# Optimization experiments

Measured on AMD Instinct MI355X. Metric: run time of the kernel, lower is better.

The kernel has to match this reference:

```python
import math
import jax, jax.numpy as jnp
import numpy as np

DIM = 1024
QK_DIM = 200
HIDDEN = 2 * DIM  # expansion_factor = 2
N = 8192


def setup_inputs() -> dict:
    key = jax.random.key(0)
    ks = jax.random.split(key, 8)
    s = 0.02
    return {
        "x": jax.random.normal(ks[0], (N, DIM), dtype=jnp.float32),
        "W_hidden": jax.random.normal(ks[1], (DIM, 2 * HIDDEN), dtype=jnp.float32) * s,
        "b_hidden": jnp.zeros((2 * HIDDEN,), dtype=jnp.float32),
        "W_qk": jax.random.normal(ks[2], (DIM, QK_DIM), dtype=jnp.float32) * s,
        "b_qk": jnp.zeros((QK_DIM,), dtype=jnp.float32),
        "gamma": 1.0 + jax.random.normal(ks[3], (2, QK_DIM), dtype=jnp.float32) * s,
        "beta": jnp.zeros((2, QK_DIM), dtype=jnp.float32),
        "W_out": jax.random.normal(ks[4], (HIDDEN, DIM), dtype=jnp.float32) * s,
        "b_out": jnp.zeros((DIM,), dtype=jnp.float32),
    }


def reference(x, W_hidden, b_hidden, W_qk, b_qk, gamma, beta, W_out, b_out):
    # to_hidden: Linear(dim -> 2*hidden) + SiLU, then chunk into v, gate
    hid = jax.nn.silu(x @ W_hidden + b_hidden)        # [N, 2H]
    v, gate = jnp.split(hid, 2, axis=-1)              # [N, H] each
    # to_qk: Linear(dim -> qk_dim) + SiLU
    qk = jax.nn.silu(x @ W_qk + b_qk)                 # [N, qk]
    # OffsetScale (heads=2): per-head affine on the shared qk
    q = qk * gamma[0] + beta[0]                       # [N, qk]
    k = qk * gamma[1] + beta[1]                       # [N, qk]
    # scores scaled by sqrt(dim) (module uses self.dim, not qk_dim)
    sim = (q @ k.T) * (1.0 / math.sqrt(x.shape[-1]))  # [N, N]
    # ReLU-squared attention (no softmax); dropout=0.0 -> identity
    attn = jnp.square(jax.nn.relu(sim))
    out = attn @ v                                    # [N, H]
    out = out * gate
    out = out @ W_out + b_out                         # [N, dim]
    # add_residual=True in this module multiplies by x
    return out * x
```

## Files before the change

kernel.cpp:

```cpp
#include <hip/hip_runtime.h>
#include <stdint.h>


typedef __bf16 bf16x8 __attribute__((ext_vector_type(8)));
typedef float f32x4 __attribute__((ext_vector_type(4)));

__device__ __forceinline__ uint16_t f2bf(float f) {
  uint32_t u = __builtin_bit_cast(uint32_t, f);
  u += 0x7fffu + ((u >> 16) & 1u);
  return (uint16_t)(u >> 16);
}
__device__ __forceinline__ float silu_f(float s) {
  return s / (1.f + __expf(-s));
}

__device__ __forceinline__ void gload16(const void* g, void* l) {
  __builtin_amdgcn_global_load_lds(
      (__attribute__((address_space(1))) void*)const_cast<void*>(g),
      (__attribute__((address_space(3))) void*)l, 16, 0, 0);
}


__global__ void cast_to_bf16(const float* __restrict__ in, uint16_t* __restrict__ out, int n4) {
  int i = blockIdx.x * blockDim.x + threadIdx.x;
  if (i < n4) {
    float4 f = ((const float4*)in)[i];
    ushort4 o;
    o.x = f2bf(f.x); o.y = f2bf(f.y); o.z = f2bf(f.z); o.w = f2bf(f.w);
    ((ushort4*)out)[i] = o;
  }
}

__global__ void transpose_cast_pad(const float* __restrict__ in, uint16_t* __restrict__ out,
                                   int R, int C, int Cp) {
  __shared__ float tile[32][33];
  int cb = blockIdx.x * 32;
  int rb = blockIdx.y * 32;
  int tx = threadIdx.x;
  int ty = threadIdx.y;
#pragma unroll
  for (int i = 0; i < 4; ++i) {
    int r = rb + ty + i * 8;
    int c = cb + tx;
    tile[ty + i * 8][tx] = (c < C) ? in[(size_t)r * C + c] : 0.f;
  }
  __syncthreads();
#pragma unroll
  for (int i = 0; i < 4; ++i) {
    int c = cb + ty + i * 8;
    if (c < Cp) out[(size_t)c * R + rb + tx] = f2bf(tile[tx][ty + i * 8]);
  }
}


struct EpiParams {
  const float* bias;
  const float* bias2;
  const float* g0;
  const float* b0;
  const float* g1;
  const float* b1;
  const uint16_t* gate;
  const float* x;
  uint16_t* o16a;
  uint16_t* o16b;
  uint16_t* oq;
  uint16_t* ok;
  float* o32;
};

#define TILE128(T_, B_, BS_)                                                   \
  do {                                                                         \
    const uint16_t* base_ = SH + (B_) * 8192;                                  \
    const int kp_ = (((T_) + 3) & (NT - 1)) * 32;                              \
    uint16_t* sd_ = SH + (BS_) * 8192 + wave * 512;                            \
    gload16(gA0 + kp_, sd_);                                                   \
    gload16(gA1 + kp_, sd_ + 2048);                                            \
    gload16(gB0 + kp_, sd_ + 4096);                                            \
    gload16(gB1 + kp_, sd_ + 6144);                                            \
    bf16x8 a_[4], b_[4];                                                       \
    _Pragma("unroll") for (int j = 0; j < 4; ++j)                              \
        b_[j] = *(const bf16x8*)(base_ + rdB + j * 512);                       \
    _Pragma("unroll") for (int i = 0; i < 4; ++i)                              \
        a_[i] = *(const bf16x8*)(base_ + rdA + i * 512);                       \
    __builtin_amdgcn_s_setprio(1);                                             \
    _Pragma("unroll") for (int i = 0; i < 4; ++i)                              \
      _Pragma("unroll") for (int j = 0; j < 4; ++j)                            \
          acc[i][j] = __builtin_amdgcn_mfma_f32_16x16x32_bf16(                 \
              a_[i], b_[j], acc[i][j], 0, 0, 0);                               \
    __builtin_amdgcn_s_setprio(0);                                             \
    asm volatile("s_waitcnt vmcnt(8)" ::: "memory");                           \
    __builtin_amdgcn_sched_barrier(0);                                         \
    __builtin_amdgcn_s_barrier();                                              \
    __builtin_amdgcn_sched_barrier(0);                                         \
  } while (0)

#define RING_LOOP128()                                                         \
  do {                                                                         \
    _Pragma("unroll") for (int s_ = 0; s_ < 3; ++s_) {                         \
      uint16_t* d_ = SH + s_ * 8192 + wave * 512;                              \
      gload16(gA0 + s_ * 32, d_);                                              \
      gload16(gA1 + s_ * 32, d_ + 2048);                                       \
      gload16(gB0 + s_ * 32, d_ + 4096);                                       \
      gload16(gB1 + s_ * 32, d_ + 6144);                                       \
    }                                                                          \
    asm volatile("s_waitcnt vmcnt(8)" ::: "memory");                           \
    __builtin_amdgcn_sched_barrier(0);                                         \
    __builtin_amdgcn_s_barrier();                                              \
    __builtin_amdgcn_sched_barrier(0);                                         \
    for (int t0_ = 0; t0_ < NT; t0_ += 4) {                                    \
      TILE128(t0_ + 0, 0, 3);                                                  \
      TILE128(t0_ + 1, 1, 0);                                                  \
      TILE128(t0_ + 2, 2, 1);                                                  \
      TILE128(t0_ + 3, 3, 2);                                                  \
    }                                                                          \
    asm volatile("s_waitcnt vmcnt(0)" ::: "memory");                           \
    __builtin_amdgcn_sched_barrier(0);                                         \
    __syncthreads();                                                           \
  } while (0)

__global__ __launch_bounds__(256, 2) void k_hidqk(
    const uint16_t* __restrict__ A, const uint16_t* __restrict__ Bt, EpiParams p) {
  __shared__ __align__(16) uint16_t SH[32768];

  const int tid = threadIdx.x;
  const int lane = tid & 63;
  const int wave = tid >> 6;
  const int wr = (wave >> 1) * 64;
  const int wc = (wave & 1) * 64;
  const int m0 = blockIdx.y * 128;
  const int n0 = blockIdx.x * 128;
  const int lda = 1024, ldb = 1024;
  const int NT = 32;

  f32x4 acc[4][4] = {};

  const int fr = lane & 15;
  const int rg = lane >> 4;
  const int swz = (rg ^ ((fr >> 1) & 3)) * 8;
  const int rdA = (wr + fr) * 32 + swz;
  const int rdB = 4096 + (wc + fr) * 32 + swz;

  const int srow = lane >> 2;
  const int sk = ((lane & 3) ^ ((lane >> 3) & 3)) * 8;
  const uint16_t* gA0 = A + (size_t)(m0 + wave * 16 + srow) * lda + sk;
  const uint16_t* gA1 = gA0 + (size_t)64 * lda;
  const uint16_t* gB0 = Bt + (size_t)(n0 + wave * 16 + srow) * ldb + sk;
  const uint16_t* gB1 = gB0 + (size_t)64 * ldb;

  RING_LOOP128();

  if (n0 < 2048) {
    uint16_t* ar = SH + wave * 2048;
    const int lrow = lane >> 3;
    const int mc = (lane & 7) * 8;
#pragma unroll
    for (int j = 0; j < 4; ++j) {
      const float bc = p.bias[n0 + wc + j * 16 + fr];
#pragma unroll
      for (int i = 0; i < 4; ++i)
#pragma unroll
        for (int r = 0; r < 4; ++r)
          ar[fr * 72 + i * 16 + rg * 4 + r] = f2bf(silu_f(acc[i][j][r] + bc));
#pragma unroll
      for (int rr = 0; rr < 2; ++rr) {
        bf16x8 v = *(const bf16x8*)(ar + (rr * 8 + lrow) * 72 + mc);
        *(bf16x8*)(p.o16a + (size_t)(n0 + wc + j * 16 + rr * 8 + lrow) * 8192 + m0 + wr + mc) = v;
      }
    }
  } else if (n0 < 4096) {
    uint16_t* ar = SH + wave * 2048;
    const int lrow = lane >> 3;
    const int nc = (lane & 7) * 8;
    float bc[4];
#pragma unroll
    for (int j = 0; j < 4; ++j) bc[j] = p.bias[n0 + wc + j * 16 + fr];
#pragma unroll
    for (int i = 0; i < 4; ++i) {
#pragma unroll
      for (int j = 0; j < 4; ++j)
#pragma unroll
        for (int r = 0; r < 4; ++r)
          ar[(rg * 4 + r) * 72 + j * 16 + fr] = f2bf(silu_f(acc[i][j][r] + bc[j]));
#pragma unroll
      for (int rr = 0; rr < 2; ++rr) {
        bf16x8 v = *(const bf16x8*)(ar + (rr * 8 + lrow) * 72 + nc);
        *(bf16x8*)(p.o16b + (size_t)(m0 + wr + i * 16 + rr * 8 + lrow) * 2048 + (n0 - 2048) + wc + nc) = v;
      }
    }
  } else {
#pragma unroll
    for (int i = 0; i < 4; ++i) {
#pragma unroll
      for (int j = 0; j < 4; ++j) {
        const int row = m0 + wr + i * 16 + rg * 4;
        const int qc = n0 + wc + j * 16 + fr - 4096;
#pragma unroll
        for (int r = 0; r < 4; ++r) {
          float qv = 0.f, kv = 0.f;
          if (qc < 200) {
            float s = silu_f(acc[i][j][r] + p.bias2[qc]);
            qv = s * p.g0[qc] + p.b0[qc];
            kv = s * p.g1[qc] + p.b1[qc];
          }
          p.oq[(size_t)(row + r) * 256 + qc] = f2bf(qv);
          p.ok[(size_t)(row + r) * 256 + qc] = f2bf(kv);
        }
      }
    }
  }
}

__global__ __launch_bounds__(256, 2) void k_attn(
    const uint16_t* __restrict__ Q,
    const uint16_t* __restrict__ Kt,
    uint16_t* __restrict__ attn) {
  __shared__ __align__(16) uint16_t SH[32768];

  const int tid = threadIdx.x;
  const int lane = tid & 63;
  const int wave = tid >> 6;
  const int wr = (wave >> 1) * 64;
  const int wc = (wave & 1) * 64;
  const int m0 = blockIdx.y * 128;
  const int n0 = blockIdx.x * 128;
  const int lda = 256, ldb = 256;
  const int NT = 8;

  f32x4 acc[4][4] = {};

  const int fr = lane & 15;
  const int rg = lane >> 4;
  const int swz = (rg ^ ((fr >> 1) & 3)) * 8;
  const int rdA = (wr + fr) * 32 + swz;
  const int rdB = 4096 + (wc + fr) * 32 + swz;

  const int srow = lane >> 2;
  const int sk = ((lane & 3) ^ ((lane >> 3) & 3)) * 8;
  const uint16_t* gA0 = Q + (size_t)(m0 + wave * 16 + srow) * lda + sk;
  const uint16_t* gA1 = gA0 + (size_t)64 * lda;
  const uint16_t* gB0 = Kt + (size_t)(n0 + wave * 16 + srow) * ldb + sk;
  const uint16_t* gB1 = gB0 + (size_t)64 * ldb;

  RING_LOOP128();

#pragma unroll
  for (int i = 0; i < 4; ++i) {
    uint16_t* sl = SH + wave * 4096 + (i & 1) * 2048;
#pragma unroll
    for (int j = 0; j < 4; ++j)
#pragma unroll
      for (int r = 0; r < 4; ++r) {
        float s = fmaxf(acc[i][j][r] * 0.03125f, 0.f);
        sl[(rg * 4 + r) * 72 + j * 16 + fr] = f2bf(s * s);
      }
    const int row = lane >> 2;
    const int c0 = (lane & 3) * 16;
    bf16x8 v0 = *(const bf16x8*)(sl + row * 72 + c0);
    bf16x8 v1 = *(const bf16x8*)(sl + row * 72 + c0 + 8);
    uint16_t* dst = attn + (size_t)(m0 + wr + i * 16 + row) * 8192 + (n0 + wc + c0);
    *(bf16x8*)(dst) = v0;
    *(bf16x8*)(dst + 8) = v1;
  }
}

__global__ __launch_bounds__(512, 2) void k_pv(
    const uint16_t* __restrict__ A, int lda,
    const uint16_t* __restrict__ Bt, int ldb,
    int K, int nx, EpiParams p) {
  __shared__ __align__(16) uint16_t SH[49152];

  const int id = blockIdx.x;
  const int bx = (id >> 3) % nx;
  const int by = (id & 7) + 8 * (id / (8 * nx));
  const int m0 = by * 128;
  const int n0 = bx * 256;

  const int tid = threadIdx.x;
  const int lane = tid & 63;
  const int wave = tid >> 6;
  const int wrM = (wave >> 2) * 64;
  const int wcN = (wave & 3) * 64;

  const int fr = lane & 15;
  const int rg = lane >> 4;
  const int swz = (rg ^ ((fr >> 1) & 3)) * 8;

  const int rdA = (wrM + fr) * 32 + swz;
  const int rdB = 4096 + (wcN + fr) * 32 + swz;

  const int srow = lane >> 2;
  const int sk = ((lane & 3) ^ ((lane >> 3) & 3)) * 8;
  const uint16_t* gA0 = A + (size_t)(m0 + wave * 16 + srow) * lda + sk;
  const uint16_t* gB0 = Bt + (size_t)(n0 + wave * 32 + srow) * ldb + sk;
  const uint16_t* gB1 = gB0 + (size_t)16 * ldb;

  f32x4 acc[4][4] = {};
  const int NT = K >> 5;

  for (int s = 0; s < 3; ++s) {
    const int ko = s * 32;
    uint16_t* d = SH + s * 12288;
    gload16(gA0 + ko, d + wave * 512);
    gload16(gB0 + ko, d + 4096 + wave * 1024);
    gload16(gB1 + ko, d + 4096 + wave * 1024 + 512);
  }
  asm volatile("s_waitcnt vmcnt(3)" ::: "memory");
  __builtin_amdgcn_sched_barrier(0);
  __builtin_amdgcn_s_barrier();
  __builtin_amdgcn_sched_barrier(0);

  bf16x8 fa0[4], fb0[4], fa1[4], fb1[4];
#pragma unroll
  for (int j = 0; j < 4; ++j) fb0[j] = *(const bf16x8*)(SH + rdB + j * 512);
#pragma unroll
  for (int i = 0; i < 4; ++i) fa0[i] = *(const bf16x8*)(SH + rdA + i * 512);

#define PV_T(T_, RS_, WS_, CA_, CB_, NA_, NB_)                                 \
  do {                                                                         \
    const int kp_ = (((T_) + 3) & (NT - 1)) * 32;                              \
    uint16_t* sd_ = SH + (WS_) * 12288;                                        \
    gload16(gA0 + kp_, sd_ + wave * 512);                                      \
    gload16(gB0 + kp_, sd_ + 4096 + wave * 1024);                              \
    gload16(gB1 + kp_, sd_ + 4096 + wave * 1024 + 512);                        \
    const uint16_t* rb_ = SH + (RS_) * 12288;                                  \
    _Pragma("unroll") for (int j = 0; j < 4; ++j)                              \
        NB_[j] = *(const bf16x8*)(rb_ + rdB + j * 512);                        \
    _Pragma("unroll") for (int i = 0; i < 4; ++i)                              \
        NA_[i] = *(const bf16x8*)(rb_ + rdA + i * 512);                        \
    __builtin_amdgcn_sched_barrier(0);                                         \
    __builtin_amdgcn_s_setprio(1);                                             \
    _Pragma("unroll") for (int i = 0; i < 4; ++i)                              \
      _Pragma("unroll") for (int j = 0; j < 4; ++j)                            \
          acc[i][j] = __builtin_amdgcn_mfma_f32_16x16x32_bf16(                 \
              CA_[i], CB_[j], acc[i][j], 0, 0, 0);                             \
    __builtin_amdgcn_s_setprio(0);                                             \
    asm volatile("s_waitcnt vmcnt(3)" ::: "memory");                           \
    __builtin_amdgcn_sched_barrier(0);                                         \
    __builtin_amdgcn_s_barrier();                                              \
    __builtin_amdgcn_sched_barrier(0);                                         \
  } while (0)

  for (int t0 = 0; t0 < NT; t0 += 4) {
    PV_T(t0 + 0, 1, 3, fa0, fb0, fa1, fb1);
    PV_T(t0 + 1, 2, 0, fa1, fb1, fa0, fb0);
    PV_T(t0 + 2, 3, 1, fa0, fb0, fa1, fb1);
    PV_T(t0 + 3, 0, 2, fa1, fb1, fa0, fb0);
  }
#undef PV_T

  asm volatile("s_waitcnt vmcnt(0)" ::: "memory");
  __builtin_amdgcn_sched_barrier(0);
  __builtin_amdgcn_s_barrier();
  __builtin_amdgcn_sched_barrier(0);

  uint16_t* ar = SH + wave * 2048;
  const int lrow = lane >> 3;
  const int nc = (lane & 7) * 8;
#pragma unroll
  for (int i = 0; i < 4; ++i) {
#pragma unroll
    for (int j = 0; j < 4; ++j)
#pragma unroll
      for (int r = 0; r < 4; ++r)
        ar[(rg * 4 + r) * 72 + j * 16 + fr] = f2bf(acc[i][j][r]);
#pragma unroll
    for (int rr = 0; rr < 2; ++rr) {
      const size_t base = (size_t)(m0 + wrM + i * 16 + rr * 8 + lrow) * 2048 + n0 + wcN + nc;
      bf16x8 v = *(const bf16x8*)(ar + (rr * 8 + lrow) * 72 + nc);
      bf16x8 g = *(const bf16x8*)(p.gate + base);
      bf16x8 o;
#pragma unroll
      for (int e = 0; e < 8; ++e) o[e] = (__bf16)((float)v[e] * (float)g[e]);
      *(bf16x8*)(p.o16a + base) = o;
    }
  }
}

__global__ __launch_bounds__(256, 2) void k_final(
    const uint16_t* __restrict__ A,
    const uint16_t* __restrict__ Bt, EpiParams p) {
  __shared__ __align__(16) uint16_t SH[32768];

  const int tid = threadIdx.x;
  const int lane = tid & 63;
  const int wave = tid >> 6;
  const int wr = (wave >> 1) * 64;
  const int wc = (wave & 1) * 64;
  const int m0 = blockIdx.y * 128;
  const int n0 = blockIdx.x * 128;
  const int lda = 2048, ldb = 2048;
  const int NT = 64;

  f32x4 acc[4][4] = {};

  const int fr = lane & 15;
  const int rg = lane >> 4;
  const int swz = (rg ^ ((fr >> 1) & 3)) * 8;
  const int rdA = (wr + fr) * 32 + swz;
  const int rdB = 4096 + (wc + fr) * 32 + swz;

  const int srow = lane >> 2;
  const int sk = ((lane & 3) ^ ((lane >> 3) & 3)) * 8;
  const uint16_t* gA0 = A + (size_t)(m0 + wave * 16 + srow) * lda + sk;
  const uint16_t* gA1 = gA0 + (size_t)64 * lda;
  const uint16_t* gB0 = Bt + (size_t)(n0 + wave * 16 + srow) * ldb + sk;
  const uint16_t* gB1 = gB0 + (size_t)64 * ldb;

  RING_LOOP128();

#pragma unroll
  for (int i = 0; i < 4; ++i) {
#pragma unroll
    for (int j = 0; j < 4; ++j) {
      const int row = m0 + wr + i * 16 + rg * 4;
      const int col = n0 + wc + j * 16 + fr;
      const float bc = p.bias[col];
#pragma unroll
      for (int r = 0; r < 4; ++r) {
        size_t idx = (size_t)(row + r) * 1024 + col;
        p.o32[idx] = (acc[i][j][r] + bc) * p.x[idx];
      }
    }
  }
}


extern "C" void kernel_launch(void* const* d_in, const int* in_sizes, int n_in,
                              void* d_out, int out_size, void* d_ws, size_t ws_size,
                              hipStream_t stream) {
  const float* x        = (const float*)d_in[0];
  const float* W_hidden = (const float*)d_in[1];
  const float* b_hidden = (const float*)d_in[2];
  const float* W_qk     = (const float*)d_in[3];
  const float* b_qk     = (const float*)d_in[4];
  const float* gamma    = (const float*)d_in[5];
  const float* beta     = (const float*)d_in[6];
  const float* W_out    = (const float*)d_in[7];
  const float* b_out    = (const float*)d_in[8];
  float* out = (float*)d_out;

  const bool fullM = ws_size >= (236ull << 20);
  const size_t region0 = fullM ? (128ull << 20) : (64ull << 20);

  char* base = (char*)d_ws;
  uint16_t* xb    = (uint16_t*)(base);
  uint16_t* WhT   = (uint16_t*)(base + (16ull << 20));
  uint16_t* WqkT  = (uint16_t*)(base + (24ull << 20));
  uint16_t* attnB = (uint16_t*)(base);
  char* tail = base + region0;
  uint16_t* WoT   = (uint16_t*)(tail);
  uint16_t* q     = (uint16_t*)(tail + (4ull << 20));
  uint16_t* kk    = (uint16_t*)(tail + (8ull << 20));
  uint16_t* vT    = (uint16_t*)(tail + (12ull << 20));
  uint16_t* gate  = (uint16_t*)(tail + (44ull << 20));
  uint16_t* out2g = (uint16_t*)(tail + (76ull << 20));
  (void)in_sizes; (void)n_in; (void)out_size;

  cast_to_bf16<<<(8192 * 1024 / 4) / 256, 256, 0, stream>>>(x, xb, 8192 * 1024 / 4);
  transpose_cast_pad<<<dim3(4096 / 32, 1024 / 32), dim3(32, 8), 0, stream>>>(W_hidden, WhT, 1024, 4096, 4096);
  transpose_cast_pad<<<dim3(256 / 32, 1024 / 32), dim3(32, 8), 0, stream>>>(W_qk, WqkT, 1024, 200, 256);
  transpose_cast_pad<<<dim3(1024 / 32, 2048 / 32), dim3(32, 8), 0, stream>>>(W_out, WoT, 2048, 1024, 1024);

  {
    EpiParams p{};
    p.bias = b_hidden; p.bias2 = b_qk;
    p.g0 = gamma; p.b0 = beta; p.g1 = gamma + 200; p.b1 = beta + 200;
    p.o16a = vT; p.o16b = gate; p.oq = q; p.ok = kk;
    k_hidqk<<<dim3(34, 64), 256, 0, stream>>>(xb, WhT, p);
  }

  if (fullM) {
    k_attn<<<dim3(64, 64), 256, 0, stream>>>(q, kk, attnB);
    {
      EpiParams p{};
      p.gate = gate; p.o16a = out2g;
      k_pv<<<dim3(8 * 64), 512, 0, stream>>>(attnB, 8192, vT, 8192, 8192, 8, p);
    }
  } else {
    for (int s = 0; s < 2; ++s) {
      k_attn<<<dim3(64, 32), 256, 0, stream>>>(q + (size_t)s * 4096 * 256, kk, attnB);
      {
        EpiParams p{};
        p.gate = gate + (size_t)s * 4096 * 2048;
        p.o16a = out2g + (size_t)s * 4096 * 2048;
        k_pv<<<dim3(8 * 32), 512, 0, stream>>>(attnB, 8192, vT, 8192, 8192, 8, p);
      }
    }
  }

  {
    EpiParams p{};
    p.bias = b_out; p.x = x; p.o32 = out;
    k_final<<<dim3(8, 64), 256, 0, stream>>>(out2g, WoT, p);
  }
}
```

Measured before the change: 604.3 us.

## Fuse QK scores and PV matmul into one flash-style kernel

Replaces the separate score kernel, which wrote the full 8192x8192 bf16 attention matrix to global memory, and the PV GEMM that read it back, with one fused kernel. Each block keeps a 64-row Q tile in LDS, computes a 128-column score tile, applies relu-squared, stages it in LDS and multiplies it by V right away, accumulating 64x1024 outputs. This removes the large attention-matrix write and read. In exchange there are only 256 blocks, K and V fragments are loaded straight from global memory without LDS staging or prefetch, and QK^T is recomputed for each of the two output halves.

```diff
diff --git a/kernel.cpp b/kernel.cpp
--- a/kernel.cpp
+++ b/kernel.cpp
@@ -211,170 +211,119 @@
   }
 }
 
-__global__ __launch_bounds__(256, 2) void k_attn(
-    const uint16_t* __restrict__ Q,
-    const uint16_t* __restrict__ Kt,
-    uint16_t* __restrict__ attn) {
-  __shared__ __align__(16) uint16_t SH[32768];
+__global__ __launch_bounds__(512, 2) void k_gau(
+    const uint16_t* __restrict__ Qg,
+    const uint16_t* __restrict__ Kg,
+    const uint16_t* __restrict__ Vt,
+    const uint16_t* __restrict__ gate,
+    uint16_t* __restrict__ out2) {
+  __shared__ __align__(16) uint16_t SH[30720];
+
+  const int id = blockIdx.x;
+  const int nch = id & 1;
+  const int mb = id >> 1;
+  const int m0 = mb * 64;
+  const int n0 = nch * 1024;
 
   const int tid = threadIdx.x;
   const int lane = tid & 63;
-  const int wave = tid >> 6;
-  const int wr = (wave >> 1) * 64;
-  const int wc = (wave & 1) * 64;
-  const int m0 = blockIdx.y * 128;
-  const int n0 = blockIdx.x * 128;
-  const int lda = 256, ldb = 256;
-  const int NT = 8;
-
-  f32x4 acc[4][4] = {};
-
+  const int w = tid >> 6;
   const int fr = lane & 15;
   const int rg = lane >> 4;
   const int swz = (rg ^ ((fr >> 1) & 3)) * 8;
-  const int rdA = (wr + fr) * 32 + swz;
-  const int rdB = 4096 + (wc + fr) * 32 + swz;
-
-  const int srow = lane >> 2;
-  const int sk = ((lane & 3) ^ ((lane >> 3) & 3)) * 8;
-  const uint16_t* gA0 = Q + (size_t)(m0 + wave * 16 + srow) * lda + sk;
-  const uint16_t* gA1 = gA0 + (size_t)64 * lda;
-  const uint16_t* gB0 = Kt + (size_t)(n0 + wave * 16 + srow) * ldb + sk;
-  const uint16_t* gB1 = gB0 + (size_t)64 * ldb;
-
-  RING_LOOP128();
-
-#pragma unroll
-  for (int i = 0; i < 4; ++i) {
-    uint16_t* sl = SH + wave * 4096 + (i & 1) * 2048;
-#pragma unroll
-    for (int j = 0; j < 4; ++j)
+
+  {
+    const int srow = lane >> 2;
+    const int sk = ((lane & 3) ^ ((lane >> 3) & 3)) * 8;
+    for (int t = w; t < 28; t += 8) {
+      const int s = t >> 2, wg = t & 3;
+      gload16(Qg + (size_t)(m0 + wg * 16 + srow) * 256 + s * 32 + sk,
+              SH + s * 2048 + wg * 512);
+    }
+  }
+  asm volatile("s_waitcnt vmcnt(0)" ::: "memory");
+  __syncthreads();
+
+  f32x4 acc[4][8] = {};
+
+  const uint16_t* kbase = Kg + (size_t)(w * 16 + fr) * 256 + rg * 8;
+  const uint16_t* vbase = Vt + (size_t)(n0 + w * 128 + fr) * 8192 + rg * 8;
+  const int plo = (w & 1) * 2 + (fr >> 3);
+  const int pkq = (w >> 1) * 2048;
+
+#pragma unroll 1
+  for (int j = 0; j < 64; ++j) {
+    const int j0 = j * 128;
+    uint16_t* Pb = SH + 14336 + (j & 1) * 8192;
+
+    f32x4 sacc[4] = {};
+#pragma unroll
+    for (int s = 0; s < 7; ++s) {
+      bf16x8 kb = *(const bf16x8*)(kbase + (size_t)j0 * 256 + s * 32);
+#pragma unroll
+      for (int i = 0; i < 4; ++i) {
+        bf16x8 qa = *(const bf16x8*)(SH + s * 2048 + (i * 16 + fr) * 32 + swz);
+        sacc[i] = __builtin_amdgcn_mfma_f32_16x16x32_bf16(qa, kb, sacc[i], 0, 0, 0);
+      }
+    }
+#pragma unroll
+    for (int i = 0; i < 4; ++i)
 #pragma unroll
       for (int r = 0; r < 4; ++r) {
-        float s = fmaxf(acc[i][j][r] * 0.03125f, 0.f);
-        sl[(rg * 4 + r) * 72 + j * 16 + fr] = f2bf(s * s);
-      }
-    const int row = lane >> 2;
-    const int c0 = (lane & 3) * 16;
-    bf16x8 v0 = *(const bf16x8*)(sl + row * 72 + c0);
-    bf16x8 v1 = *(const bf16x8*)(sl + row * 72 + c0 + 8);
-    uint16_t* dst = attn + (size_t)(m0 + wr + i * 16 + row) * 8192 + (n0 + wc + c0);
-    *(bf16x8*)(dst) = v0;
-    *(bf16x8*)(dst + 8) = v1;
-  }
-}
-
-__global__ __launch_bounds__(512, 2) void k_pv(
-    const uint16_t* __restrict__ A, int lda,
-    const uint16_t* __restrict__ Bt, int ldb,
-    int K, int nx, EpiParams p) {
-  __shared__ __align__(16) uint16_t SH[49152];
-
-  const int id = blockIdx.x;
-  const int bx = (id >> 3) % nx;
-  const int by = (id & 7) + 8 * (id / (8 * nx));
-  const int m0 = by * 128;
-  const int n0 = bx * 256;
-
-  const int tid = threadIdx.x;
-  const int lane = tid & 63;
-  const int wave = tid >> 6;
-  const int wrM = (wave >> 2) * 64;
-  const int wcN = (wave & 3) * 64;
-
-  const int fr = lane & 15;
-  const int rg = lane >> 4;
-  const int swz = (rg ^ ((fr >> 1) & 3)) * 8;
-
-  const int rdA = (wrM + fr) * 32 + swz;
-  const int rdB = 4096 + (wcN + fr) * 32 + swz;
-
-  const int srow = lane >> 2;
-  const int sk = ((lane & 3) ^ ((lane >> 3) & 3)) * 8;
-  const uint16_t* gA0 = A + (size_t)(m0 + wave * 16 + srow) * lda + sk;
-  const uint16_t* gB0 = Bt + (size_t)(n0 + wave * 32 + srow) * ldb + sk;
-  const uint16_t* gB1 = gB0 + (size_t)16 * ldb;
-
-  f32x4 acc[4][4] = {};
-  const int NT = K >> 5;
-
-  for (int s = 0; s < 3; ++s) {
-    const int ko = s * 32;
-    uint16_t* d = SH + s * 12288;
-    gload16(gA0 + ko, d + wave * 512);
-    gload16(gB0 + ko, d + 4096 + wave * 1024);
-    gload16(gB1 + ko, d + 4096 + wave * 1024 + 512);
-  }
-  asm volatile("s_waitcnt vmcnt(3)" ::: "memory");
-  __builtin_amdgcn_sched_barrier(0);
-  __builtin_amdgcn_s_barrier();
-  __builtin_amdgcn_sched_barrier(0);
-
-  bf16x8 fa0[4], fb0[4], fa1[4], fb1[4];
-#pragma unroll
-  for (int j = 0; j < 4; ++j) fb0[j] = *(const bf16x8*)(SH + rdB + j * 512);
-#pragma unroll
-  for (int i = 0; i < 4; ++i) fa0[i] = *(const bf16x8*)(SH + rdA + i * 512);
-
-#define PV_T(T_, RS_, WS_, CA_, CB_, NA_, NB_)                                 \
-  do {                                                                         \
-    const int kp_ = (((T_) + 3) & (NT - 1)) * 32;                              \
-    uint16_t* sd_ = SH + (WS_) * 12288;                                        \
-    gload16(gA0 + kp_, sd_ + wave * 512);                                      \
-    gload16(gB0 + kp_, sd_ + 4096 + wave * 1024);                              \
-    gload16(gB1 + kp_, sd_ + 4096 + wave * 1024 + 512);                        \
-    const uint16_t* rb_ = SH + (RS_) * 12288;                                  \
-    _Pragma("unroll") for (int j = 0; j < 4; ++j)                              \
-        NB_[j] = *(const bf16x8*)(rb_ + rdB + j * 512);                        \
-    _Pragma("unroll") for (int i = 0; i < 4; ++i)                              \
-        NA_[i] = *(const bf16x8*)(rb_ + rdA + i * 512);                        \
-    __builtin_amdgcn_sched_barrier(0);                                         \
-    __builtin_amdgcn_s_setprio(1);                                             \
-    _Pragma("unroll") for (int i = 0; i < 4; ++i)                              \
-      _Pragma("unroll") for (int j = 0; j < 4; ++j)                            \
-          acc[i][j] = __builtin_amdgcn_mfma_f32_16x16x32_bf16(                 \
-              CA_[i], CB_[j], acc[i][j], 0, 0, 0);                             \
-    __builtin_amdgcn_s_setprio(0);                                             \
-    asm volatile("s_waitcnt vmcnt(3)" ::: "memory");                           \
-    __builtin_amdgcn_sched_barrier(0);                                         \
-    __builtin_amdgcn_s_barrier();                                              \
-    __builtin_amdgcn_sched_barrier(0);                                         \
-  } while (0)
-
-  for (int t0 = 0; t0 < NT; t0 += 4) {
-    PV_T(t0 + 0, 1, 3, fa0, fb0, fa1, fb1);
-    PV_T(t0 + 1, 2, 0, fa1, fb1, fa0, fb0);
-    PV_T(t0 + 2, 3, 1, fa0, fb0, fa1, fb1);
-    PV_T(t0 + 3, 0, 2, fa1, fb1, fa0, fb0);
-  }
-#undef PV_T
-
-  asm volatile("s_waitcnt vmcnt(0)" ::: "memory");
-  __builtin_amdgcn_sched_barrier(0);
-  __builtin_amdgcn_s_barrier();
-  __builtin_amdgcn_sched_barrier(0);
-
-  uint16_t* ar = SH + wave * 2048;
+        const int m = i * 16 + rg * 4 + r;
+        float sv = fmaxf(sacc[i][r] * 0.03125f, 0.f);
+        Pb[pkq + m * 32 + ((plo ^ ((m >> 1) & 3)) * 8) + (fr & 7)] = f2bf(sv * sv);
+      }
+    __syncthreads();
+
+#pragma unroll
+    for (int ks = 0; ks < 4; ++ks) {
+      bf16x8 pa[4];
+#pragma unroll
+      for (int i = 0; i < 4; ++i)
+        pa[i] = *(const bf16x8*)(Pb + ks * 2048 + (i * 16 + fr) * 32 + swz);
+#pragma unroll
+      for (int jh = 0; jh < 2; ++jh) {
+        bf16x8 vb[4];
+#pragma unroll
+        for (int jj = 0; jj < 4; ++jj)
+          vb[jj] = *(const bf16x8*)(vbase + (size_t)(jh * 64 + jj * 16) * 8192 + j0 + ks * 32);
+        __builtin_amdgcn_s_setprio(1);
+#pragma unroll
+        for (int i = 0; i < 4; ++i)
+#pragma unroll
+          for (int jj = 0; jj < 4; ++jj)
+            acc[i][jh * 4 + jj] = __builtin_amdgcn_mfma_f32_16x16x32_bf16(
+                pa[i], vb[jj], acc[i][jh * 4 + jj], 0, 0, 0);
+        __builtin_amdgcn_s_setprio(0);
+      }
+    }
+  }
+  __syncthreads();
+
+  uint16_t* ar = SH + w * 3840;
   const int lrow = lane >> 3;
-  const int nc = (lane & 7) * 8;
-#pragma unroll
-  for (int i = 0; i < 4; ++i) {
-#pragma unroll
-    for (int j = 0; j < 4; ++j)
-#pragma unroll
-      for (int r = 0; r < 4; ++r)
-        ar[(rg * 4 + r) * 72 + j * 16 + fr] = f2bf(acc[i][j][r]);
-#pragma unroll
-    for (int rr = 0; rr < 2; ++rr) {
-      const size_t base = (size_t)(m0 + wrM + i * 16 + rr * 8 + lrow) * 2048 + n0 + wcN + nc;
-      bf16x8 v = *(const bf16x8*)(ar + (rr * 8 + lrow) * 72 + nc);
-      bf16x8 g = *(const bf16x8*)(p.gate + base);
-      bf16x8 o;
-#pragma unroll
-      for (int e = 0; e < 8; ++e) o[e] = (__bf16)((float)v[e] * (float)g[e]);
-      *(bf16x8*)(p.o16a + base) = o;
-    }
-  }
+  const int nc8 = (lane & 7) * 8;
+#pragma unroll
+  for (int i = 0; i < 4; ++i)
+#pragma unroll
+    for (int h = 0; h < 2; ++h) {
+#pragma unroll
+      for (int jj = 0; jj < 4; ++jj)
+#pragma unroll
+        for (int r = 0; r < 4; ++r)
+          ar[(rg * 4 + r) * 72 + jj * 16 + fr] = f2bf(acc[i][h * 4 + jj][r]);
+#pragma unroll
+      for (int rr = 0; rr < 2; ++rr) {
+        const size_t base = (size_t)(m0 + i * 16 + rr * 8 + lrow) * 2048 + n0 + w * 128 + h * 64 + nc8;
+        bf16x8 v = *(const bf16x8*)(ar + (rr * 8 + lrow) * 72 + nc8);
+        bf16x8 g = *(const bf16x8*)(gate + base);
+        bf16x8 o;
+#pragma unroll
+        for (int e = 0; e < 8; ++e) o[e] = (__bf16)((float)v[e] * (float)g[e]);
+        *(bf16x8*)(out2 + base) = o;
+      }
+    }
 }
 
 __global__ __launch_bounds__(256, 2) void k_final(
@@ -440,22 +389,17 @@
   const float* b_out    = (const float*)d_in[8];
   float* out = (float*)d_out;
 
-  const bool fullM = ws_size >= (236ull << 20);
-  const size_t region0 = fullM ? (128ull << 20) : (64ull << 20);
-
   char* base = (char*)d_ws;
   uint16_t* xb    = (uint16_t*)(base);
   uint16_t* WhT   = (uint16_t*)(base + (16ull << 20));
   uint16_t* WqkT  = (uint16_t*)(base + (24ull << 20));
-  uint16_t* attnB = (uint16_t*)(base);
-  char* tail = base + region0;
-  uint16_t* WoT   = (uint16_t*)(tail);
-  uint16_t* q     = (uint16_t*)(tail + (4ull << 20));
-  uint16_t* kk    = (uint16_t*)(tail + (8ull << 20));
-  uint16_t* vT    = (uint16_t*)(tail + (12ull << 20));
-  uint16_t* gate  = (uint16_t*)(tail + (44ull << 20));
-  uint16_t* out2g = (uint16_t*)(tail + (76ull << 20));
-  (void)in_sizes; (void)n_in; (void)out_size;
+  uint16_t* WoT   = (uint16_t*)(base + (25ull << 20));
+  uint16_t* q     = (uint16_t*)(base + (29ull << 20));
+  uint16_t* kk    = (uint16_t*)(base + (33ull << 20));
+  uint16_t* vT    = (uint16_t*)(base + (37ull << 20));
+  uint16_t* gate  = (uint16_t*)(base + (69ull << 20));
+  uint16_t* out2g = (uint16_t*)(base + (101ull << 20));
+  (void)in_sizes; (void)n_in; (void)out_size; (void)ws_size;
 
   cast_to_bf16<<<(8192 * 1024 / 4) / 256, 256, 0, stream>>>(x, xb, 8192 * 1024 / 4);
   transpose_cast_pad<<<dim3(4096 / 32, 1024 / 32), dim3(32, 8), 0, stream>>>(W_hidden, WhT, 1024, 4096, 4096);
@@ -470,24 +414,7 @@
     k_hidqk<<<dim3(34, 64), 256, 0, stream>>>(xb, WhT, p);
   }
 
-  if (fullM) {
-    k_attn<<<dim3(64, 64), 256, 0, stream>>>(q, kk, attnB);
-    {
-      EpiParams p{};
-      p.gate = gate; p.o16a = out2g;
-      k_pv<<<dim3(8 * 64), 512, 0, stream>>>(attnB, 8192, vT, 8192, 8192, 8, p);
-    }
-  } else {
-    for (int s = 0; s < 2; ++s) {
-      k_attn<<<dim3(64, 32), 256, 0, stream>>>(q + (size_t)s * 4096 * 256, kk, attnB);
-      {
-        EpiParams p{};
-        p.gate = gate + (size_t)s * 4096 * 2048;
-        p.o16a = out2g + (size_t)s * 4096 * 2048;
-        k_pv<<<dim3(8 * 32), 512, 0, stream>>>(attnB, 8192, vT, 8192, 8192, 8, p);
-      }
-    }
-  }
+  k_gau<<<dim3(256), 512, 0, stream>>>(q, kk, vT, gate, out2g);
 
   {
     EpiParams p{};
```

After: 883.6 us. 46.2% more time.
